# Performance work log

Hardware: AMD Instinct MI355X
Metric: run time of the kernel (lower is better)

Reference implementation:

```python
import jax, jax.numpy as jnp
import numpy as np

B, C, G = 32768, 17, 7  # batch, channels (1 obj + 4 box + 12 class), grid


def setup_inputs() -> dict:
    key = jax.random.key(0)
    k1, k2, k3 = jax.random.split(key, 3)
    # Predictions: uniform in (0,1) so sqrt of wh channels is well-defined.
    out = jax.random.uniform(k1, (B, C, G, G), dtype=jnp.float32, minval=1e-4, maxval=1.0)
    # remaining channels uniform in (0,1).
    label = jax.random.uniform(k2, (B, C, G, G), dtype=jnp.float32, minval=1e-4, maxval=1.0)
    obj = (jax.random.uniform(k3, (B, 1, G, G)) < 0.3).astype(jnp.float32)
    label = label.at[:, 0:1].set(obj)
    return {"out": out, "label": label}


def reference(out, label):
    # objectness channel
    d0 = label[:, 0] - out[:, 0]                      # [B,7,7]
    noobj_loss = 0.5 * d0 ** 2
    # object-present branch
    loc_loss = jnp.sum((label[:, 1:3] - out[:, 1:3]) ** 2, axis=1)                       # [B,7,7]
    size_loss = jnp.sum((jnp.sqrt(label[:, 3:5]) - jnp.sqrt(out[:, 3:5])) ** 2, axis=1)  # [B,7,7]
    prob_loss = d0 ** 2
    class_loss = jnp.sum((label[:, 5:17] - out[:, 5:17]) ** 2, axis=1)                   # [B,7,7]
    obj_loss = 5.0 * (loc_loss + size_loss) + prob_loss + class_loss
    cell_loss = jnp.where(label[:, 0] == 0, noobj_loss, obj_loss)
    return jnp.sum(cell_loss) / (out.shape[0] * 49)
```

## Files before the change

kernel.cpp:

```cpp
#include <hip/hip_runtime.h>


#define BPC   833
#define CELLS 49
#define NTOT  (32768 * BPC)
#define N4    (NTOT / 4)
#define NBLK  2048

__global__ __launch_bounds__(256) void yolo_partial(const float* __restrict__ outp,
                                                    const float* __restrict__ lab,
                                                    float* __restrict__ partial) {
    const int tid    = blockIdx.x * 256 + threadIdx.x;
    const int stride = gridDim.x * 256;
    float acc = 0.0f;

    for (int i4 = tid; i4 < N4; i4 += stride) {
        const float4 o4 = reinterpret_cast<const float4*>(outp)[i4];
        const float4 l4 = reinterpret_cast<const float4*>(lab)[i4];
        const float ov[4] = {o4.x, o4.y, o4.z, o4.w};
        const float lv[4] = {l4.x, l4.y, l4.z, l4.w};
        const int base = i4 * 4;
#pragma unroll
        for (int j = 0; j < 4; ++j) {
            const int idx  = base + j;
            const int b    = idx / BPC;
            const int r    = idx - b * BPC;
            const int c    = r / CELLS;
            const int cell = r - c * CELLS;
            const float o1 = ov[j];
            const float l1 = lv[j];
            float contrib;
            if (c == 0) {
                const float d = l1 - o1;
                contrib = d * d * ((l1 != 0.0f) ? 1.0f : 0.5f);
            } else {
                const float m = lab[b * BPC + cell];
                const float s = (m != 0.0f) ? 1.0f : 0.0f;
                float d, w;
                if (c >= 5)      { d = l1 - o1;                     w = s;        }
                else if (c >= 3) { d = sqrtf(l1) - sqrtf(o1);       w = 5.0f * s; }
                else             { d = l1 - o1;                     w = 5.0f * s; }
                contrib = w * d * d;
            }
            acc += contrib;
        }
    }

#pragma unroll
    for (int off = 32; off > 0; off >>= 1)
        acc += __shfl_down(acc, off, 64);

    __shared__ float wsum[4];
    const int lane = threadIdx.x & 63;
    const int wid  = threadIdx.x >> 6;
    if (lane == 0) wsum[wid] = acc;
    __syncthreads();
    if (threadIdx.x == 0)
        partial[blockIdx.x] = wsum[0] + wsum[1] + wsum[2] + wsum[3];
}

__global__ __launch_bounds__(256) void yolo_final(const float* __restrict__ partial,
                                                  float* __restrict__ outv) {
    float acc = 0.0f;
    for (int i = threadIdx.x; i < NBLK; i += 256) acc += partial[i];
#pragma unroll
    for (int off = 32; off > 0; off >>= 1)
        acc += __shfl_down(acc, off, 64);

    __shared__ float wsum[4];
    const int lane = threadIdx.x & 63;
    const int wid  = threadIdx.x >> 6;
    if (lane == 0) wsum[wid] = acc;
    __syncthreads();
    if (threadIdx.x == 0)
        outv[0] = (wsum[0] + wsum[1] + wsum[2] + wsum[3]) * (1.0f / 1605632.0f);
}

extern "C" void kernel_launch(void* const* d_in, const int* in_sizes, int n_in,
                              void* d_out, int out_size, void* d_ws, size_t ws_size,
                              hipStream_t stream) {
    const float* outp = (const float*)d_in[0];
    const float* lab  = (const float*)d_in[1];
    float* partial    = (float*)d_ws;
    float* res        = (float*)d_out;

    yolo_partial<<<NBLK, 256, 0, stream>>>(outp, lab, partial);
    yolo_final<<<1, 256, 0, stream>>>(partial, res);
}
```

Measured before the change: 46.74 us.

## Map one thread per grid cell and iterate channels with strided loads

Each thread now handles one (batch, cell) pair and loops over all 17 channels, instead of handling four contiguous elements with per-element index division and a separate objectness-mask reload. The intent is to drop the integer divisions and the redundant mask loads per element, and to use m as an arithmetic weight instead of branching. The cost is scalar loads instead of float4 loads. Consecutive threads still read consecutive addresses within each channel plane, but lanes that cross a batch boundary hit a 784-float gap, so coalescing is less regular. The new code also assumes labels are exactly 0 or 1.

```diff
diff --git a/kernel.cpp b/kernel.cpp
--- a/kernel.cpp
+++ b/kernel.cpp
@@ -1,11 +1,10 @@
 #include <hip/hip_runtime.h>
 
 
-#define BPC   833
-#define CELLS 49
-#define NTOT  (32768 * BPC)
-#define N4    (NTOT / 4)
-#define NBLK  2048
+#define BPC    833
+#define CELLS  49
+#define NCELL  (32768 * CELLS)
+#define NBLK   2048
 
 __global__ __launch_bounds__(256) void yolo_partial(const float* __restrict__ outp,
                                                     const float* __restrict__ lab,
@@ -14,36 +13,34 @@
     const int stride = gridDim.x * 256;
     float acc = 0.0f;
 
-    for (int i4 = tid; i4 < N4; i4 += stride) {
-        const float4 o4 = reinterpret_cast<const float4*>(outp)[i4];
-        const float4 l4 = reinterpret_cast<const float4*>(lab)[i4];
-        const float ov[4] = {o4.x, o4.y, o4.z, o4.w};
-        const float lv[4] = {l4.x, l4.y, l4.z, l4.w};
-        const int base = i4 * 4;
+    for (int ci = tid; ci < NCELL; ci += stride) {
+        const int b    = ci / CELLS;
+        const int cell = ci - b * CELLS;
+        const float* __restrict__ lb = lab  + b * BPC + cell;
+        const float* __restrict__ ob = outp + b * BPC + cell;
+
+        const float m  = lb[0];
+        const float o0 = ob[0];
+        const float d0 = m - o0;
+
+        float loc = 0.0f, siz = 0.0f, cls = 0.0f;
 #pragma unroll
-        for (int j = 0; j < 4; ++j) {
-            const int idx  = base + j;
-            const int b    = idx / BPC;
-            const int r    = idx - b * BPC;
-            const int c    = r / CELLS;
-            const int cell = r - c * CELLS;
-            const float o1 = ov[j];
-            const float l1 = lv[j];
-            float contrib;
-            if (c == 0) {
-                const float d = l1 - o1;
-                contrib = d * d * ((l1 != 0.0f) ? 1.0f : 0.5f);
-            } else {
-                const float m = lab[b * BPC + cell];
-                const float s = (m != 0.0f) ? 1.0f : 0.0f;
-                float d, w;
-                if (c >= 5)      { d = l1 - o1;                     w = s;        }
-                else if (c >= 3) { d = sqrtf(l1) - sqrtf(o1);       w = 5.0f * s; }
-                else             { d = l1 - o1;                     w = 5.0f * s; }
-                contrib = w * d * d;
-            }
-            acc += contrib;
+        for (int c = 1; c <= 2; ++c) {
+            const float d = lb[c * CELLS] - ob[c * CELLS];
+            loc += d * d;
         }
+#pragma unroll
+        for (int c = 3; c <= 4; ++c) {
+            const float d = sqrtf(lb[c * CELLS]) - sqrtf(ob[c * CELLS]);
+            siz += d * d;
+        }
+#pragma unroll
+        for (int c = 5; c <= 16; ++c) {
+            const float d = lb[c * CELLS] - ob[c * CELLS];
+            cls += d * d;
+        }
+
+        acc += d0 * d0 * (0.5f + 0.5f * m) + m * (5.0f * (loc + siz) + cls);
     }
 
 #pragma unroll
```

New measurement: 49.10 us. +5.1%, slower.
